# Kernel tuning notes

Measured on AMD Instinct MI355X. Metric: run time of the kernel, lower is better.

Reference implementation:

```python
import jax, jax.numpy as jnp
import numpy as np

EPS = 1e-4

def setup_inputs() -> dict:
    key = jax.random.key(0)
    ks = jax.random.split(key, 8)
    B, S, D, N = 4, 4096, 1024, 256
    return {
        "tokens": jax.random.normal(ks[0], (B, S, D), dtype=jnp.float32),
        "norm_w": jnp.ones((D,), dtype=jnp.float32),
        "W_in": jax.random.normal(ks[1], (N, D), dtype=jnp.float32) * (1.0 / np.sqrt(D)),
        "b_in": jax.random.normal(ks[2], (N,), dtype=jnp.float32) * 0.02,
        "W_out": jax.random.normal(ks[3], (D, N), dtype=jnp.float32) * (1.0 / np.sqrt(N)),
        "b_out": jax.random.normal(ks[4], (D,), dtype=jnp.float32) * 0.02,
        "W_skip": jax.random.normal(ks[5], (D, D), dtype=jnp.float32) * (1.0 / np.sqrt(D)),
        "b_skip": jax.random.normal(ks[6], (D,), dtype=jnp.float32) * 0.02,
        "log_decay": jnp.zeros((N,), dtype=jnp.float32),
    }

def reference(tokens, norm_w, W_in, b_in, W_out, b_out, W_skip, b_skip, log_decay):
    # RMSNorm (eps=1e-4), matching torch nn.RMSNorm
    ms = jnp.mean(tokens * tokens, axis=-1, keepdims=True)
    x = tokens * jax.lax.rsqrt(ms + EPS) * norm_w  # [B,S,D]

    decay = jax.nn.sigmoid(log_decay)  # [N]
    u = jnp.einsum("bsd,nd->bsn", x, W_in) + b_in  # [B,S,N] input projection, batched

    def step(state, u_t):  # state [B,N], u_t [B,N]
        state = decay * state + u_t
        return state, state

    B, S, _ = x.shape
    init = jnp.zeros((B, W_in.shape[0]), dtype=x.dtype)
    _, states = jax.lax.scan(step, init, jnp.swapaxes(u, 0, 1))  # [S,B,N]
    states = jnp.swapaxes(states, 0, 1)  # [B,S,N]

    y = jnp.einsum("bsn,dn->bsd", states, W_out) + b_out
    y = y + jnp.einsum("bsd,ed->bse", x, W_skip) + b_skip
    return tokens + y
```

## Files before the change

kernel.cpp:

```cpp
#include <hip/hip_runtime.h>

typedef __bf16 bf16_t;
typedef __bf16 bf16x4 __attribute__((ext_vector_type(4)));
typedef __bf16 bf16x8 __attribute__((ext_vector_type(8)));
typedef float  f32x4  __attribute__((ext_vector_type(4)));

#define ASYNC_COPY16(gp, lp)                                                     \
  __builtin_amdgcn_global_load_lds(                                              \
      (const __attribute__((address_space(1))) void*)(gp),                       \
      (__attribute__((address_space(3))) void*)(lp), 16, 0, 0)

__global__ __launch_bounds__(256) void k_cvt_all(const float* __restrict__ s0,
                                                 bf16_t* __restrict__ d0,
                                                 const float* __restrict__ s1,
                                                 bf16_t* __restrict__ d1,
                                                 const float* __restrict__ s2,
                                                 bf16_t* __restrict__ d2) {
  const int bid = blockIdx.x;
  const float* s;
  bf16_t* d;
  int i;
  if (bid < 256)      { s = s0; d = d0; i = bid * 256 + threadIdx.x; }
  else if (bid < 512) { s = s1; d = d1; i = (bid - 256) * 256 + threadIdx.x; }
  else                { s = s2; d = d2; i = (bid - 512) * 256 + threadIdx.x; }
  float4 v = ((const float4*)s)[i];
  bf16x4 o;
  o[0] = (bf16_t)v.x; o[1] = (bf16_t)v.y; o[2] = (bf16_t)v.z; o[3] = (bf16_t)v.w;
  ((bf16x4*)d)[i] = o;
}

__global__ __launch_bounds__(256) void k_rmsnorm(const float* __restrict__ tokens,
                                                 const float* __restrict__ norm_w,
                                                 bf16_t* __restrict__ x) {
  const int row = blockIdx.x;
  const int tid = threadIdx.x;
  const size_t base = (size_t)row * 1024;
  float4 v = ((const float4*)(tokens + base))[tid];
  float ss = v.x * v.x + v.y * v.y + v.z * v.z + v.w * v.w;
#pragma unroll
  for (int off = 32; off > 0; off >>= 1) ss += __shfl_down(ss, off);
  __shared__ float sred[4];
  if ((tid & 63) == 0) sred[tid >> 6] = ss;
  __syncthreads();
  float tot = sred[0] + sred[1] + sred[2] + sred[3];
  float scale = rsqrtf(tot * (1.0f / 1024.0f) + 1e-4f);
  float4 wv = ((const float4*)norm_w)[tid];
  bf16x4 o;
  o[0] = (bf16_t)(v.x * scale * wv.x);
  o[1] = (bf16_t)(v.y * scale * wv.y);
  o[2] = (bf16_t)(v.z * scale * wv.z);
  o[3] = (bf16_t)(v.w * scale * wv.w);
  *(bf16x4*)(x + base + (size_t)tid * 4) = o;
}

__global__ __launch_bounds__(256, 4) void k_gemm1(const bf16_t* __restrict__ A,
                                                  const bf16_t* __restrict__ Bw,
                                                  const float* __restrict__ bias,
                                                  float* __restrict__ C) {
  constexpr int K = 1024, Nc = 256;
  __shared__ __align__(16) bf16_t sA[64 * 64];
  __shared__ __align__(16) bf16_t sB[64 * 64];
  const int tid = threadIdx.x;
  const int lane = tid & 63;
  const int w = tid >> 6;
  const int wm = w >> 1, wn = w & 1;

  const int bid = blockIdx.x;
  const int swz = (bid & 7) * 128 + (bid >> 3);
  const int bm = swz >> 2;
  const int bn = swz & 3;

  const int st_row = tid >> 3;
  const int st_col = ((tid & 7) ^ ((tid >> 3) & 7)) * 8;
  const int lds_off = tid * 8;

  f32x4 acc[2][2] = {};

  for (int k0 = 0; k0 < K; k0 += 64) {
#pragma unroll
    for (int j = 0; j < 2; ++j)
      ASYNC_COPY16(A + (size_t)(bm * 64 + j * 32 + st_row) * K + k0 + st_col,
                   &sA[j * 2048 + lds_off]);
#pragma unroll
    for (int j = 0; j < 2; ++j)
      ASYNC_COPY16(Bw + (size_t)(bn * 64 + j * 32 + st_row) * K + k0 + st_col,
                   &sB[j * 2048 + lds_off]);
    asm volatile("s_waitcnt vmcnt(0)" ::: "memory");
    __syncthreads();

#pragma unroll
    for (int kk = 0; kk < 2; ++kk) {
      const int slot = ((kk * 4 + (lane >> 4)) ^ (lane & 7)) * 8;
      bf16x8 af[2], bfr[2];
#pragma unroll
      for (int m = 0; m < 2; ++m)
        af[m] = *(const bf16x8*)&sA[(wm * 32 + m * 16 + (lane & 15)) * 64 + slot];
#pragma unroll
      for (int n = 0; n < 2; ++n)
        bfr[n] = *(const bf16x8*)&sB[(wn * 32 + n * 16 + (lane & 15)) * 64 + slot];
#pragma unroll
      for (int m = 0; m < 2; ++m)
#pragma unroll
        for (int n = 0; n < 2; ++n)
          acc[m][n] = __builtin_amdgcn_mfma_f32_16x16x32_bf16(af[m], bfr[n],
                                                              acc[m][n], 0, 0, 0);
    }
    __syncthreads();
  }

#pragma unroll
  for (int n = 0; n < 2; ++n) {
    const int col = bn * 64 + wn * 32 + n * 16 + (lane & 15);
    const float bv = bias[col];
#pragma unroll
    for (int m = 0; m < 2; ++m) {
      const int rbase = bm * 64 + wm * 32 + m * 16 + (lane >> 4) * 4;
#pragma unroll
      for (int j = 0; j < 4; ++j)
        C[(size_t)(rbase + j) * Nc + col] = acc[m][n][j] + bv;
    }
  }
}

__global__ __launch_bounds__(256) void k_scan(const float* __restrict__ u,
                                              const float* __restrict__ log_decay,
                                              bf16_t* __restrict__ states) {
  const int n = threadIdx.x;
  const int c = blockIdx.x;
  const int b = blockIdx.y;
  const float decay = 1.0f / (1.0f + __expf(-log_decay[n]));
  const float* up = u + (size_t)b * 4096 * 256 + n;
  bf16_t* sp = states + (size_t)b * 4096 * 256 + n;
  const int t0 = c * 64;
  const int tb = (c == 0) ? 0 : t0 - 64;
  const int te = t0 + 64;
  float state = 0.0f;
  for (int tblk = tb; tblk < te; tblk += 8) {
    float v[8];
#pragma unroll
    for (int q = 0; q < 8; ++q) v[q] = up[(size_t)(tblk + q) * 256];
#pragma unroll
    for (int q = 0; q < 8; ++q) {
      state = fmaf(decay, state, v[q]);
      if (tblk + q >= t0) sp[(size_t)(tblk + q) * 256] = (bf16_t)state;
    }
  }
}

__global__ __launch_bounds__(512, 2) void k_gemm2(const bf16_t* __restrict__ St,
                                                  const bf16_t* __restrict__ X,
                                                  const bf16_t* __restrict__ Wo,
                                                  const bf16_t* __restrict__ Wsk,
                                                  const float* __restrict__ tokens,
                                                  const float* __restrict__ b_out,
                                                  const float* __restrict__ b_skip,
                                                  float* __restrict__ out) {
  __shared__ __align__(16) bf16_t sA[2][2 * 128 * 64];
  __shared__ __align__(16) bf16_t sB[2][2 * 128 * 64];
  const int tid = threadIdx.x;
  const int lane = tid & 63;
  const int w = tid >> 6;
  const int wm = w >> 2;
  const int wn = w & 3;

  const int bid = blockIdx.x;
  const int swz = (bid & 7) * 32 + (bid >> 3);
  const int bm = swz >> 2;
  const int bn = swz & 3;

  const int st_row = w * 8 + (lane >> 3);
  const int st_col = ((lane & 7) ^ (lane >> 3)) * 8;
  const int lds_off = w * 512 + lane * 8;

  f32x4 acc[8][4] = {};

  auto stage_half = [&](int kt, int q) {
    const int h = q & 1;
    const bf16_t* src;
    int ld, kb;
    if (q < 2) {
      if (kt < 4) { src = St; ld = 256;  kb = kt * 64; }
      else        { src = X;  ld = 1024; kb = (kt - 4) * 64; }
      src += (size_t)(bm * 256 + h * 128 + st_row) * ld + kb + st_col;
      bf16_t* l = &sA[kt & 1][h * 8192 + lds_off];
#pragma unroll
      for (int j = 0; j < 2; ++j)
        ASYNC_COPY16(src + (size_t)(j * 64) * ld, l + j * 4096);
    } else {
      if (kt < 4) { src = Wo;  ld = 256;  kb = kt * 64; }
      else        { src = Wsk; ld = 1024; kb = (kt - 4) * 64; }
      src += (size_t)(bn * 256 + h * 128 + st_row) * ld + kb + st_col;
      bf16_t* l = &sB[kt & 1][h * 8192 + lds_off];
#pragma unroll
      for (int j = 0; j < 2; ++j)
        ASYNC_COPY16(src + (size_t)(j * 64) * ld, l + j * 4096);
    }
  };

#pragma unroll
  for (int q = 0; q < 4; ++q) stage_half(0, q);

  const int bhalf = wn >> 1;
  const int brow0 = (wn & 1) * 64;

  for (int t = 0; t < 20; ++t) {
    asm volatile("s_waitcnt vmcnt(0)" ::: "memory");
    __builtin_amdgcn_sched_barrier(0);
    __builtin_amdgcn_s_barrier();
    __builtin_amdgcn_sched_barrier(0);

    const bf16_t* a = &sA[t & 1][wm * 8192];
    const bf16_t* b = &sB[t & 1][bhalf * 8192];

#pragma unroll
    for (int mh = 0; mh < 2; ++mh) {
      bf16x8 af[4][2];
#pragma unroll
      for (int m = 0; m < 4; ++m)
#pragma unroll
        for (int kk = 0; kk < 2; ++kk) {
          const int slot = ((kk * 4 + (lane >> 4)) ^ (lane & 7)) * 8;
          af[m][kk] = *(const bf16x8*)
              &a[((mh * 4 + m) * 16 + (lane & 15)) * 64 + slot];
        }
#pragma unroll
      for (int nh = 0; nh < 2; ++nh) {
        if (t < 19) stage_half(t + 1, mh * 2 + nh);
        bf16x8 bfr[2][2];
#pragma unroll
        for (int n = 0; n < 2; ++n)
#pragma unroll
          for (int kk = 0; kk < 2; ++kk) {
            const int slot = ((kk * 4 + (lane >> 4)) ^ (lane & 7)) * 8;
            bfr[n][kk] = *(const bf16x8*)
                &b[(brow0 + (nh * 2 + n) * 16 + (lane & 15)) * 64 + slot];
          }
        __builtin_amdgcn_s_setprio(1);
#pragma unroll
        for (int m = 0; m < 4; ++m)
#pragma unroll
          for (int n = 0; n < 2; ++n)
#pragma unroll
            for (int kk = 0; kk < 2; ++kk)
              acc[mh * 4 + m][nh * 2 + n] = __builtin_amdgcn_mfma_f32_16x16x32_bf16(
                  af[m][kk], bfr[n][kk], acc[mh * 4 + m][nh * 2 + n], 0, 0, 0);
        __builtin_amdgcn_s_setprio(0);
      }
    }
  }

  const int row0 = bm * 256 + wm * 128 + (lane >> 4) * 4;
  const int col0 = bn * 256 + wn * 64 + (lane & 15);
#pragma unroll
  for (int n = 0; n < 4; ++n) {
    const int col = col0 + n * 16;
    const float bv = b_out[col] + b_skip[col];
#pragma unroll
    for (int m = 0; m < 8; ++m) {
      const int r = row0 + m * 16;
#pragma unroll
      for (int j = 0; j < 4; ++j) {
        const size_t idx = (size_t)(r + j) * 1024 + col;
        out[idx] = acc[m][n][j] + tokens[idx] + bv;
      }
    }
  }
}

extern "C" void kernel_launch(void* const* d_in, const int* in_sizes, int n_in,
                              void* d_out, int out_size, void* d_ws, size_t ws_size,
                              hipStream_t stream) {
  const float* tokens  = (const float*)d_in[0];
  const float* norm_w  = (const float*)d_in[1];
  const float* W_in    = (const float*)d_in[2];
  const float* b_in    = (const float*)d_in[3];
  const float* W_out   = (const float*)d_in[4];
  const float* b_out   = (const float*)d_in[5];
  const float* W_skip  = (const float*)d_in[6];
  const float* b_skip  = (const float*)d_in[7];
  const float* log_dec = (const float*)d_in[8];
  float* out = (float*)d_out;

  char* w = (char*)d_ws;
  bf16_t* xb  = (bf16_t*)(w);
  float*  u   = (float*)(w + 33554432ull);
  bf16_t* st  = (bf16_t*)(w + 50331648ull);
  bf16_t* Wi  = (bf16_t*)(w + 58720256ull);
  bf16_t* Wo  = (bf16_t*)(w + 59244544ull);
  bf16_t* Wsk = (bf16_t*)(w + 59768832ull);

  k_cvt_all<<<dim3(1536), 256, 0, stream>>>(W_in, Wi, W_out, Wo, W_skip, Wsk);

  k_rmsnorm<<<dim3(16384), 256, 0, stream>>>(tokens, norm_w, xb);

  k_gemm1<<<dim3(1024), 256, 0, stream>>>(xb, Wi, b_in, u);

  k_scan<<<dim3(64, 4), 256, 0, stream>>>(u, log_dec, st);

  k_gemm2<<<dim3(256), 512, 0, stream>>>(st, xb, Wo, Wsk, tokens, b_out,
                                         b_skip, out);
}
```

Baseline: 152.2 us.

## Fuse prep kernels, store u as bf16, and deepen gemm2 pipeline

Merges the weight conversion and RMSNorm into a single launch, which removes one kernel launch. The gemm1 output u is now stored in bf16, halving the traffic for its write and for the scan's read, at some cost in precision of the recurrence input. gemm2 is restructured to a two-stage-ahead prefetch with partial vmcnt waits and quarter-tile MFMA phases, so global loads overlap compute better. gemm1 also drops its explicit vmcnt wait before the barrier, which risks reading LDS before the async copies have landed.

```diff
diff --git a/kernel.cpp b/kernel.cpp
--- a/kernel.cpp
+++ b/kernel.cpp
@@ -10,30 +10,31 @@
       (const __attribute__((address_space(1))) void*)(gp),                       \
       (__attribute__((address_space(3))) void*)(lp), 16, 0, 0)
 
-__global__ __launch_bounds__(256) void k_cvt_all(const float* __restrict__ s0,
-                                                 bf16_t* __restrict__ d0,
-                                                 const float* __restrict__ s1,
-                                                 bf16_t* __restrict__ d1,
-                                                 const float* __restrict__ s2,
-                                                 bf16_t* __restrict__ d2) {
+__global__ __launch_bounds__(256) void k_prep(const float* __restrict__ tokens,
+                                              const float* __restrict__ norm_w,
+                                              bf16_t* __restrict__ x,
+                                              const float* __restrict__ W_in,
+                                              bf16_t* __restrict__ Wi,
+                                              const float* __restrict__ W_out,
+                                              bf16_t* __restrict__ Wo,
+                                              const float* __restrict__ W_skip,
+                                              bf16_t* __restrict__ Wsk) {
   const int bid = blockIdx.x;
-  const float* s;
-  bf16_t* d;
-  int i;
-  if (bid < 256)      { s = s0; d = d0; i = bid * 256 + threadIdx.x; }
-  else if (bid < 512) { s = s1; d = d1; i = (bid - 256) * 256 + threadIdx.x; }
-  else                { s = s2; d = d2; i = (bid - 512) * 256 + threadIdx.x; }
-  float4 v = ((const float4*)s)[i];
-  bf16x4 o;
-  o[0] = (bf16_t)v.x; o[1] = (bf16_t)v.y; o[2] = (bf16_t)v.z; o[3] = (bf16_t)v.w;
-  ((bf16x4*)d)[i] = o;
-}
-
-__global__ __launch_bounds__(256) void k_rmsnorm(const float* __restrict__ tokens,
-                                                 const float* __restrict__ norm_w,
-                                                 bf16_t* __restrict__ x) {
-  const int row = blockIdx.x;
   const int tid = threadIdx.x;
+  if (bid < 1536) {
+    const float* s;
+    bf16_t* d;
+    int i;
+    if (bid < 256)      { s = W_in;   d = Wi;  i = bid * 256 + tid; }
+    else if (bid < 512) { s = W_out;  d = Wo;  i = (bid - 256) * 256 + tid; }
+    else                { s = W_skip; d = Wsk; i = (bid - 512) * 256 + tid; }
+    float4 v = ((const float4*)s)[i];
+    bf16x4 o;
+    o[0] = (bf16_t)v.x; o[1] = (bf16_t)v.y; o[2] = (bf16_t)v.z; o[3] = (bf16_t)v.w;
+    ((bf16x4*)d)[i] = o;
+    return;
+  }
+  const int row = bid - 1536;
   const size_t base = (size_t)row * 1024;
   float4 v = ((const float4*)(tokens + base))[tid];
   float ss = v.x * v.x + v.y * v.y + v.z * v.z + v.w * v.w;
@@ -56,7 +57,7 @@
 __global__ __launch_bounds__(256, 4) void k_gemm1(const bf16_t* __restrict__ A,
                                                   const bf16_t* __restrict__ Bw,
                                                   const float* __restrict__ bias,
-                                                  float* __restrict__ C) {
+                                                  bf16_t* __restrict__ C) {
   constexpr int K = 1024, Nc = 256;
   __shared__ __align__(16) bf16_t sA[64 * 64];
   __shared__ __align__(16) bf16_t sB[64 * 64];
@@ -85,7 +86,6 @@
     for (int j = 0; j < 2; ++j)
       ASYNC_COPY16(Bw + (size_t)(bn * 64 + j * 32 + st_row) * K + k0 + st_col,
                    &sB[j * 2048 + lds_off]);
-    asm volatile("s_waitcnt vmcnt(0)" ::: "memory");
     __syncthreads();
 
 #pragma unroll
@@ -117,19 +117,19 @@
       const int rbase = bm * 64 + wm * 32 + m * 16 + (lane >> 4) * 4;
 #pragma unroll
       for (int j = 0; j < 4; ++j)
-        C[(size_t)(rbase + j) * Nc + col] = acc[m][n][j] + bv;
-    }
-  }
-}
-
-__global__ __launch_bounds__(256) void k_scan(const float* __restrict__ u,
+        C[(size_t)(rbase + j) * Nc + col] = (bf16_t)(acc[m][n][j] + bv);
+    }
+  }
+}
+
+__global__ __launch_bounds__(256) void k_scan(const bf16_t* __restrict__ u,
                                               const float* __restrict__ log_decay,
                                               bf16_t* __restrict__ states) {
   const int n = threadIdx.x;
   const int c = blockIdx.x;
   const int b = blockIdx.y;
   const float decay = 1.0f / (1.0f + __expf(-log_decay[n]));
-  const float* up = u + (size_t)b * 4096 * 256 + n;
+  const bf16_t* up = u + (size_t)b * 4096 * 256 + n;
   bf16_t* sp = states + (size_t)b * 4096 * 256 + n;
   const int t0 = c * 64;
   const int tb = (c == 0) ? 0 : t0 - 64;
@@ -138,7 +138,7 @@
   for (int tblk = tb; tblk < te; tblk += 8) {
     float v[8];
 #pragma unroll
-    for (int q = 0; q < 8; ++q) v[q] = up[(size_t)(tblk + q) * 256];
+    for (int q = 0; q < 8; ++q) v[q] = (float)up[(size_t)(tblk + q) * 256];
 #pragma unroll
     for (int q = 0; q < 8; ++q) {
       state = fmaf(decay, state, v[q]);
@@ -155,8 +155,8 @@
                                                   const float* __restrict__ b_out,
                                                   const float* __restrict__ b_skip,
                                                   float* __restrict__ out) {
-  __shared__ __align__(16) bf16_t sA[2][2 * 128 * 64];
-  __shared__ __align__(16) bf16_t sB[2][2 * 128 * 64];
+  __shared__ __align__(16) bf16_t sA[2][2][128 * 64];
+  __shared__ __align__(16) bf16_t sB[2][2][128 * 64];
   const int tid = threadIdx.x;
   const int lane = tid & 63;
   const int w = tid >> 6;
@@ -168,85 +168,140 @@
   const int bm = swz >> 2;
   const int bn = swz & 3;
 
-  const int st_row = w * 8 + (lane >> 3);
-  const int st_col = ((lane & 7) ^ (lane >> 3)) * 8;
-  const int lds_off = w * 512 + lane * 8;
+  const int st_row = tid >> 3;
+  const int st_scol = ((tid & 7) ^ ((tid >> 3) & 7)) * 8;
+  const int st_off = tid * 8;
 
   f32x4 acc[8][4] = {};
 
-  auto stage_half = [&](int kt, int q) {
-    const int h = q & 1;
-    const bf16_t* src;
+  auto srcA = [&](int kt, int& ld, int& kb) -> const bf16_t* {
+    if (kt < 4) { ld = 256;  kb = kt * 64;       return St; }
+    else        { ld = 1024; kb = (kt - 4) * 64; return X;  }
+  };
+  auto srcB = [&](int kt, int& ld, int& kb) -> const bf16_t* {
+    if (kt < 4) { ld = 256;  kb = kt * 64;       return Wo;  }
+    else        { ld = 1024; kb = (kt - 4) * 64; return Wsk; }
+  };
+
+  auto stageA = [&](int kt) {
     int ld, kb;
-    if (q < 2) {
-      if (kt < 4) { src = St; ld = 256;  kb = kt * 64; }
-      else        { src = X;  ld = 1024; kb = (kt - 4) * 64; }
-      src += (size_t)(bm * 256 + h * 128 + st_row) * ld + kb + st_col;
-      bf16_t* l = &sA[kt & 1][h * 8192 + lds_off];
-#pragma unroll
-      for (int j = 0; j < 2; ++j)
-        ASYNC_COPY16(src + (size_t)(j * 64) * ld, l + j * 4096);
-    } else {
-      if (kt < 4) { src = Wo;  ld = 256;  kb = kt * 64; }
-      else        { src = Wsk; ld = 1024; kb = (kt - 4) * 64; }
-      src += (size_t)(bn * 256 + h * 128 + st_row) * ld + kb + st_col;
-      bf16_t* l = &sB[kt & 1][h * 8192 + lds_off];
-#pragma unroll
-      for (int j = 0; j < 2; ++j)
-        ASYNC_COPY16(src + (size_t)(j * 64) * ld, l + j * 4096);
+    const bf16_t* s = srcA(kt, ld, kb);
+#pragma unroll
+    for (int h = 0; h < 2; ++h) {
+      const bf16_t* g = s + (size_t)(bm * 256 + h * 128 + st_row) * ld + kb + st_scol;
+      bf16_t* l = &sA[kt & 1][h][st_off];
+      ASYNC_COPY16(g, l);
+      ASYNC_COPY16(g + (size_t)64 * ld, l + 4096);
     }
   };
-
-#pragma unroll
-  for (int q = 0; q < 4; ++q) stage_half(0, q);
-
-  const int bhalf = wn >> 1;
+  auto stageB = [&](int kt) {
+    int ld, kb;
+    const bf16_t* s = srcB(kt, ld, kb);
+#pragma unroll
+    for (int h = 0; h < 2; ++h) {
+      const bf16_t* g = s + (size_t)(bn * 256 + h * 128 + st_row) * ld + kb + st_scol;
+      bf16_t* l = &sB[kt & 1][h][st_off];
+      ASYNC_COPY16(g, l);
+      ASYNC_COPY16(g + (size_t)64 * ld, l + 4096);
+    }
+  };
+
+  stageA(0); stageB(0);
+  stageA(1); stageB(1);
+
   const int brow0 = (wn & 1) * 64;
 
-  for (int t = 0; t < 20; ++t) {
-    asm volatile("s_waitcnt vmcnt(0)" ::: "memory");
-    __builtin_amdgcn_sched_barrier(0);
-    __builtin_amdgcn_s_barrier();
-    __builtin_amdgcn_sched_barrier(0);
-
-    const bf16_t* a = &sA[t & 1][wm * 8192];
-    const bf16_t* b = &sB[t & 1][bhalf * 8192];
-
-#pragma unroll
-    for (int mh = 0; mh < 2; ++mh) {
-      bf16x8 af[4][2];
-#pragma unroll
-      for (int m = 0; m < 4; ++m)
-#pragma unroll
-        for (int kk = 0; kk < 2; ++kk) {
-          const int slot = ((kk * 4 + (lane >> 4)) ^ (lane & 7)) * 8;
-          af[m][kk] = *(const bf16x8*)
-              &a[((mh * 4 + m) * 16 + (lane & 15)) * 64 + slot];
-        }
-#pragma unroll
-      for (int nh = 0; nh < 2; ++nh) {
-        if (t < 19) stage_half(t + 1, mh * 2 + nh);
-        bf16x8 bfr[2][2];
-#pragma unroll
-        for (int n = 0; n < 2; ++n)
-#pragma unroll
-          for (int kk = 0; kk < 2; ++kk) {
-            const int slot = ((kk * 4 + (lane >> 4)) ^ (lane & 7)) * 8;
-            bfr[n][kk] = *(const bf16x8*)
-                &b[(brow0 + (nh * 2 + n) * 16 + (lane & 15)) * 64 + slot];
-          }
-        __builtin_amdgcn_s_setprio(1);
-#pragma unroll
-        for (int m = 0; m < 4; ++m)
-#pragma unroll
-          for (int n = 0; n < 2; ++n)
-#pragma unroll
-            for (int kk = 0; kk < 2; ++kk)
-              acc[mh * 4 + m][nh * 2 + n] = __builtin_amdgcn_mfma_f32_16x16x32_bf16(
-                  af[m][kk], bfr[n][kk], acc[mh * 4 + m][nh * 2 + n], 0, 0, 0);
-        __builtin_amdgcn_s_setprio(0);
-      }
-    }
+  for (int kt = 0; kt < 20; ++kt) {
+    const bf16_t* a = &sA[kt & 1][wm][0];
+    const bf16_t* b = &sB[kt & 1][wn >> 1][0];
+
+    bf16x8 af[4][2], bf0[2][2], bf1[2][2];
+
+    if (kt < 19) asm volatile("s_waitcnt vmcnt(8)" ::: "memory");
+    else         asm volatile("s_waitcnt vmcnt(0)" ::: "memory");
+    __builtin_amdgcn_s_barrier();
+    asm volatile("" ::: "memory");
+#pragma unroll
+    for (int m = 0; m < 4; ++m)
+#pragma unroll
+      for (int kk = 0; kk < 2; ++kk) {
+        const int slot = ((kk * 4 + (lane >> 4)) ^ (lane & 7)) * 8;
+        af[m][kk] = *(const bf16x8*)&a[(m * 16 + (lane & 15)) * 64 + slot];
+      }
+#pragma unroll
+    for (int n = 0; n < 2; ++n)
+#pragma unroll
+      for (int kk = 0; kk < 2; ++kk) {
+        const int slot = ((kk * 4 + (lane >> 4)) ^ (lane & 7)) * 8;
+        bf0[n][kk] = *(const bf16x8*)&b[(brow0 + n * 16 + (lane & 15)) * 64 + slot];
+      }
+    __builtin_amdgcn_s_setprio(1);
+#pragma unroll
+    for (int m = 0; m < 4; ++m)
+#pragma unroll
+      for (int n = 0; n < 2; ++n)
+#pragma unroll
+        for (int kk = 0; kk < 2; ++kk)
+          acc[m][n] = __builtin_amdgcn_mfma_f32_16x16x32_bf16(af[m][kk], bf0[n][kk],
+                                                              acc[m][n], 0, 0, 0);
+    __builtin_amdgcn_s_setprio(0);
+    __builtin_amdgcn_s_barrier();
+    asm volatile("" ::: "memory");
+
+#pragma unroll
+    for (int n = 0; n < 2; ++n)
+#pragma unroll
+      for (int kk = 0; kk < 2; ++kk) {
+        const int slot = ((kk * 4 + (lane >> 4)) ^ (lane & 7)) * 8;
+        bf1[n][kk] = *(const bf16x8*)&b[(brow0 + (2 + n) * 16 + (lane & 15)) * 64 + slot];
+      }
+    __builtin_amdgcn_s_setprio(1);
+#pragma unroll
+    for (int m = 0; m < 4; ++m)
+#pragma unroll
+      for (int n = 0; n < 2; ++n)
+#pragma unroll
+        for (int kk = 0; kk < 2; ++kk)
+          acc[m][2 + n] = __builtin_amdgcn_mfma_f32_16x16x32_bf16(af[m][kk], bf1[n][kk],
+                                                                  acc[m][2 + n], 0, 0, 0);
+    __builtin_amdgcn_s_setprio(0);
+    __builtin_amdgcn_s_barrier();
+    asm volatile("" ::: "memory");
+
+    if (kt < 18) stageB(kt + 2);
+#pragma unroll
+    for (int m = 0; m < 4; ++m)
+#pragma unroll
+      for (int kk = 0; kk < 2; ++kk) {
+        const int slot = ((kk * 4 + (lane >> 4)) ^ (lane & 7)) * 8;
+        af[m][kk] = *(const bf16x8*)&a[((4 + m) * 16 + (lane & 15)) * 64 + slot];
+      }
+    __builtin_amdgcn_s_setprio(1);
+#pragma unroll
+    for (int m = 0; m < 4; ++m)
+#pragma unroll
+      for (int n = 0; n < 2; ++n)
+#pragma unroll
+        for (int kk = 0; kk < 2; ++kk)
+          acc[4 + m][2 + n] = __builtin_amdgcn_mfma_f32_16x16x32_bf16(af[m][kk], bf1[n][kk],
+                                                                      acc[4 + m][2 + n], 0, 0, 0);
+    __builtin_amdgcn_s_setprio(0);
+    __builtin_amdgcn_s_barrier();
+    asm volatile("" ::: "memory");
+
+    if (kt < 18) stageA(kt + 2);
+    __builtin_amdgcn_s_setprio(1);
+#pragma unroll
+    for (int m = 0; m < 4; ++m)
+#pragma unroll
+      for (int n = 0; n < 2; ++n)
+#pragma unroll
+        for (int kk = 0; kk < 2; ++kk)
+          acc[4 + m][n] = __builtin_amdgcn_mfma_f32_16x16x32_bf16(af[m][kk], bf0[n][kk],
+                                                                  acc[4 + m][n], 0, 0, 0);
+    __builtin_amdgcn_s_setprio(0);
+    __builtin_amdgcn_s_barrier();
+    asm volatile("" ::: "memory");
   }
 
   const int row0 = bm * 256 + wm * 128 + (lane >> 4) * 4;
@@ -283,15 +338,14 @@
 
   char* w = (char*)d_ws;
   bf16_t* xb  = (bf16_t*)(w);
-  float*  u   = (float*)(w + 33554432ull);
-  bf16_t* st  = (bf16_t*)(w + 50331648ull);
-  bf16_t* Wi  = (bf16_t*)(w + 58720256ull);
-  bf16_t* Wo  = (bf16_t*)(w + 59244544ull);
-  bf16_t* Wsk = (bf16_t*)(w + 59768832ull);
-
-  k_cvt_all<<<dim3(1536), 256, 0, stream>>>(W_in, Wi, W_out, Wo, W_skip, Wsk);
-
-  k_rmsnorm<<<dim3(16384), 256, 0, stream>>>(tokens, norm_w, xb);
+  bf16_t* u   = (bf16_t*)(w + 33554432ull);
+  bf16_t* st  = (bf16_t*)(w + 41943040ull);
+  bf16_t* Wi  = (bf16_t*)(w + 50331648ull);
+  bf16_t* Wo  = (bf16_t*)(w + 50855936ull);
+  bf16_t* Wsk = (bf16_t*)(w + 51380224ull);
+
+  k_prep<<<dim3(17920), 256, 0, stream>>>(tokens, norm_w, xb, W_in, Wi,
+                                          W_out, Wo, W_skip, Wsk);
 
   k_gemm1<<<dim3(1024), 256, 0, stream>>>(xb, Wi, b_in, u);
 
```

After: 142.9 us. 6.1% less time.
